# Performance work log

Hardware: AMD Instinct MI355X
Metric: run time of the kernel (lower is better)

Reference implementation:

```python
import jax, jax.numpy as jnp
import numpy as np

NEG_BIG = -9.0e15  # matches torch's -9000000000000000.0
LEAKY_SLOPE = 0.01  # nn.LeakyReLU default


def setup_inputs() -> dict:
    key = jax.random.key(0)
    k1, k2, k3, k4, k5, k6 = jax.random.split(key, 6)
    B, N, NEMB, NHID = 1, 8192, 128, 64
    x = jax.random.normal(k1, (B, N, NEMB), dtype=jnp.float32)
    adj = jax.random.randint(k2, (B, N, N), 0, 2, dtype=jnp.int32)
    # learned parameters (xavier-ish scale)
    w_weight = jax.random.normal(k3, (NHID, NEMB), dtype=jnp.float32) * (1.0 / np.sqrt(NEMB))
    w_bias = jnp.zeros((NHID,), dtype=jnp.float32)
    a_weight = jax.random.normal(k4, (1, 2 * NHID), dtype=jnp.float32) * (1.0 / np.sqrt(2 * NHID))
    a_bias = jnp.zeros((1,), dtype=jnp.float32)
    return {"x": x, "adj": adj, "w_weight": w_weight, "w_bias": w_bias,
            "a_weight": a_weight, "a_bias": a_bias}


def reference(x, adj, w_weight, w_bias, a_weight, a_bias):
    # h = W x + b : [B, N, F]
    h = jnp.einsum("bnd,fd->bnf", x, w_weight) + w_bias
    F = h.shape[-1]
    # The torch code forms a[b,i,j] = concat(h_i, h_j) then Linear(2F->1).
    # Equivalent decomposition avoids the [B,N,N,2F] tensor:
    # e[b,i,j] = leaky_relu(h_i . a_src + h_j . a_dst + a_bias)
    a_src, a_dst = a_weight[0, :F], a_weight[0, F:]
    s_src = jnp.einsum("bnf,f->bn", h, a_src)  # [B, N]
    s_dst = jnp.einsum("bnf,f->bn", h, a_dst)  # [B, N]
    e = jax.nn.leaky_relu(s_src[:, :, None] + s_dst[:, None, :] + a_bias[0],
                          negative_slope=LEAKY_SLOPE)  # [B, N, N]
    # masked_scatter_ semantics: True positions (row-major over the WHOLE
    # flattened tensor) receive e's elements taken sequentially in order.
    mask_flat = (adj > 0).reshape(-1)
    take_idx = jnp.cumsum(mask_flat.astype(jnp.int32)) - 1  # position in source stream
    src_flat = e.reshape(-1)
    att = jnp.where(mask_flat, src_flat[take_idx], jnp.float32(NEG_BIG)).reshape(e.shape)
    # softmax over dim=2, dropout in eval mode (identity)
    att = jax.nn.softmax(att, axis=2)
    out = jax.nn.elu(jnp.einsum("bij,bjf->bif", att, h))  # [B, N, F]
    return out
```

## Files before the change

### kernel.cpp

```cpp
#include <hip/hip_runtime.h>
#include <cstdint>
#include <cstddef>

#define N 8192
#define F 64
#define NEMB 128
#define BI 16
#define BJ 256
#define NCHUNK 32
#define HALFCH 16
#define ROWSTR 560
#define LEAKY 0.01f

typedef __attribute__((ext_vector_type(8))) short bf16x8;
typedef __attribute__((ext_vector_type(4))) float f32x4;

__device__ __forceinline__ float wave_reduce_sum_f(float v){
  #pragma unroll
  for (int d = 32; d > 0; d >>= 1) v += __shfl_xor(v, d, 64);
  return v;
}
__device__ __forceinline__ int wave_reduce_sum_i(int v){
  #pragma unroll
  for (int d = 32; d > 0; d >>= 1) v += __shfl_xor(v, d, 64);
  return v;
}
__device__ __forceinline__ int wave_incl_scan_i(int v, int lane){
  #pragma unroll
  for (int d = 1; d < 64; d <<= 1){
    int u = __shfl_up(v, d, 64);
    if (lane >= d) v += u;
  }
  return v;
}
__device__ __forceinline__ unsigned short f2bf(float x){
  union { float f; unsigned u; } v; v.f = x;
  unsigned r = v.u + 0x7fff + ((v.u >> 16) & 1);
  return (unsigned short)(r >> 16);
}

extern "C" __global__ void __launch_bounds__(256)
k_packh(const int* __restrict__ adj, unsigned short* __restrict__ bm,
        unsigned short* __restrict__ ccnt, int* __restrict__ rowtot,
        const float* __restrict__ x, const float* __restrict__ ww,
        const float* __restrict__ wb, const float* __restrict__ aw,
        float* __restrict__ h, float* __restrict__ ssrc, float* __restrict__ sdst2x){
  const int t = threadIdx.x;
  if (blockIdx.x < N){
    const int i = blockIdx.x;
    int total = 0;
    #pragma unroll
    for (int half = 0; half < 2; ++half){
      const int w = half*256 + t;
      const int4* p4 = (const int4*)(adj + (size_t)i*N + w*16);
      unsigned m = 0;
      #pragma unroll
      for (int k = 0; k < 4; ++k){
        int4 a = p4[k];
        m |= (unsigned)(a.x>0) << (k*4+0);
        m |= (unsigned)(a.y>0) << (k*4+1);
        m |= (unsigned)(a.z>0) << (k*4+2);
        m |= (unsigned)(a.w>0) << (k*4+3);
      }
      bm[((size_t)(w>>4)*N + i)*16 + (w&15)] = (unsigned short)m;
      const int pc = __popc(m);
      total += pc;
      int cs = pc;
      cs += __shfl_xor(cs, 1, 16);
      cs += __shfl_xor(cs, 2, 16);
      cs += __shfl_xor(cs, 4, 16);
      cs += __shfl_xor(cs, 8, 16);
      if ((t & 15) == 0) ccnt[(size_t)i*NCHUNK + (w>>4)] = (unsigned short)cs;
    }
    total = wave_reduce_sum_i(total);
    __shared__ int ws_[4];
    if ((t & 63) == 0) ws_[t >> 6] = total;
    __syncthreads();
    if (t == 0) rowtot[i] = ws_[0] + ws_[1] + ws_[2] + ws_[3];
  } else {
    const int w = t >> 6, lane = t & 63;
    __shared__ float xs[4][NEMB];
    const int n0 = (blockIdx.x - N) * 4;
    ((float2*)&xs[0][0])[t] = ((const float2*)(x + (size_t)n0 * NEMB))[t];
    __syncthreads();
    const int n = n0 + w;
    const float4* w4 = (const float4*)(ww + (size_t)lane * NEMB);
    const float4* x4 = (const float4*)&xs[w][0];
    float acc = wb[lane];
    #pragma unroll
    for (int k = 0; k < NEMB/4; ++k){
      float4 a = x4[k]; float4 b = w4[k];
      acc = fmaf(a.x, b.x, acc);
      acc = fmaf(a.y, b.y, acc);
      acc = fmaf(a.z, b.z, acc);
      acc = fmaf(a.w, b.w, acc);
    }
    h[(size_t)n * F + lane] = acc;
    float vs = wave_reduce_sum_f(acc * aw[lane]);
    float vd = wave_reduce_sum_f(acc * aw[F + lane]);
    if (lane == 0){ ssrc[n] = vs; sdst2x[n] = vd; sdst2x[n + N] = vd; }
  }
}

extern "C" __global__ void __launch_bounds__(256)
k_tr(const float* __restrict__ h, unsigned short* __restrict__ ht){
  __shared__ float tile[64][65];
  const int t = threadIdx.x;
  const int n0 = blockIdx.x * 64;
  #pragma unroll
  for (int s = 0; s < 4; ++s){
    const int r = s*16 + (t>>4);
    const int c = (t&15)*4;
    const float4 v = *(const float4*)(h + (size_t)(n0+r)*F + c);
    tile[r][c] = v.x; tile[r][c+1] = v.y; tile[r][c+2] = v.z; tile[r][c+3] = v.w;
  }
  __syncthreads();
  const int f = t >> 2, jq = t & 3;
  unsigned short buf[16];
  #pragma unroll
  for (int k = 0; k < 16; ++k) buf[k] = f2bf(tile[jq*16 + k][f]);
  *(uint4*)(ht + (size_t)f*N + n0 + jq*16)     = *(uint4*)&buf[0];
  *(uint4*)(ht + (size_t)f*N + n0 + jq*16 + 8) = *(uint4*)&buf[8];
}

extern "C" __global__ void __launch_bounds__(1024)
k_scan(const int* __restrict__ cnt, int* __restrict__ base){
  __shared__ int wsum[16];
  const int t = threadIdx.x, lane = t & 63, w = t >> 6;
  int4 aa = ((const int4*)cnt)[t * 2];
  int4 bb = ((const int4*)cnt)[t * 2 + 1];
  int v[8] = {aa.x, aa.y, aa.z, aa.w, bb.x, bb.y, bb.z, bb.w};
  int local = 0;
  #pragma unroll
  for (int k = 0; k < 8; ++k){ int tmp = v[k]; v[k] = local; local += tmp; }
  int inc = wave_incl_scan_i(local, lane);
  int wexcl = inc - local;
  if (lane == 63) wsum[w] = inc;
  __syncthreads();
  if (t == 0){
    int run = 0;
    #pragma unroll
    for (int k = 0; k < 16; ++k){ int tmp = wsum[k]; wsum[k] = run; run += tmp; }
  }
  __syncthreads();
  const int b0 = wsum[w] + wexcl;
  ((int4*)base)[t * 2]     = make_int4(b0 + v[0], b0 + v[1], b0 + v[2], b0 + v[3]);
  ((int4*)base)[t * 2 + 1] = make_int4(b0 + v[4], b0 + v[5], b0 + v[6], b0 + v[7]);
}

extern "C" __global__ void __launch_bounds__(256, 4)
k_main(const unsigned short* __restrict__ bm, const unsigned short* __restrict__ ccnt,
       const int* __restrict__ base, const unsigned short* __restrict__ ht,
       const float* __restrict__ ssrc, const float* __restrict__ sdst2x,
       const float* __restrict__ abias,
       float* __restrict__ pnum, float* __restrict__ pden){
  __shared__ __attribute__((aligned(16))) char pt[2][16*ROWSTR];
  __shared__ unsigned short ccum[BI][HALFCH];
  __shared__ int basel[BI];

  const int t = threadIdx.x, w = t >> 6, lane = t & 63;
  const int vid = blockIdx.x >> 1, half = blockIdx.x & 1;
  const int i0 = vid * BI;
  const int ch0 = half * HALFCH;

  if (t < BI) basel[t] = base[i0 + t];
  {
    const int r = t >> 4, g = t & 15;
    int c = (int)ccnt[(size_t)(i0+r)*NCHUNK + ch0 + g];
    int pre = 0;
    if (half){
      pre = (int)ccnt[(size_t)(i0+r)*NCHUNK + g];
      #pragma unroll
      for (int d = 1; d < 16; d <<= 1) pre += __shfl_xor(pre, d, 16);
    }
    int inc = c;
    #pragma unroll
    for (int d = 1; d < 16; d <<= 1){ int u = __shfl_up(inc, d, 16); if (g >= d) inc += u; }
    ccum[r][g] = (unsigned short)(pre + inc - c);
  }
  __syncthreads();

  const int r = t >> 4, g = t & 15;
  const int fr = lane & 15, ks = lane >> 4;
  const int fB = w*16 + fr;
  char* buf0 = pt[0];
  char* buf1 = pt[1];
  const float ab = abias[0];
  const int rowbase = basel[r];
  float dsum = 0.f;
  f32x4 acc = {0.f, 0.f, 0.f, 0.f};
  bf16x8 bregA[8], bregB[8];

#define PREFETCH(CH, BR) { \
    const unsigned short* hBp = ht + (size_t)fB*N + (CH)*BJ + ks*8; \
    _Pragma("unroll") \
    for (int kk = 0; kk < 8; ++kk) BR[kk] = *(const bf16x8*)(hBp + kk*32); \
    __builtin_amdgcn_sched_barrier(0); \
  }

#define PRODUCE(CC, PB) { \
    const int cc_ = (CC); \
    const int ch = ch0 + cc_; \
    const unsigned m = (unsigned)bm[((size_t)ch*N + (i0+r))*16 + g]; \
    const int c = __popc(m); \
    int inc = c; \
    _Pragma("unroll") \
    for (int d = 1; d < 16; d <<= 1){ int u = __shfl_up(inc, d, 16); if (g >= d) inc += u; } \
    const int qex = inc - c; \
    const int q0row = rowbase + (int)ccum[r][cc_]; \
    const float* sdw = sdst2x + (q0row & (N - 1)) + qex; \
    const int ilo = q0row >> 13; \
    const float s_lo = ssrc[ilo]; \
    const float s_hi = ssrc[ilo + 1]; \
    const int krel = ((ilo + 1) << 13) - q0row - qex; \
    char* myrow = (PB) + r*ROWSTR; \
    *(uint4*)(myrow + g*32)      = make_uint4(0,0,0,0); \
    *(uint4*)(myrow + g*32 + 16) = make_uint4(0,0,0,0); \
    float wv[16]; \
    _Pragma("unroll") \
    for (int k = 0; k < 16; ++k) wv[k] = sdw[k]; \
    unsigned mc = m; \
    _Pragma("unroll") \
    for (int k = 0; k < 16; ++k){ \
      const float ss = (k >= krel) ? s_hi : s_lo; \
      float e = ss + wv[k] + ab; \
      e = (e > 0.f) ? e : LEAKY * e; \
      const float p = __expf(e); \
      const int pos = __ffs(mc) - 1; \
      const bool act = (k < c); \
      dsum += act ? p : 0.f; \
      const int off = act ? (g*32 + pos*2) : (512 + g*2); \
      *(unsigned short*)(myrow + off) = f2bf(p); \
      mc &= mc - 1; \
    } \
  }

#define MM(PB, BR) { \
    const char* aP = (PB) + fr*ROWSTR; \
    __builtin_amdgcn_s_setprio(1); \
    _Pragma("unroll") \
    for (int kk = 0; kk < 8; ++kk){ \
      bf16x8 av = *(const bf16x8*)(aP + kk*64 + ks*16); \
      acc = __builtin_amdgcn_mfma_f32_16x16x32_bf16(av, BR[kk], acc, 0, 0, 0); \
    } \
    __builtin_amdgcn_s_setprio(0); \
  }

  PREFETCH(ch0, bregA)
  PRODUCE(0, buf0)
  __syncthreads();
  for (int cc = 0; cc < HALFCH; cc += 2){
    PREFETCH(ch0 + cc + 1, bregB)
    PRODUCE(cc + 1, buf1)
    MM(buf0, bregA)
    __syncthreads();
    if (cc + 2 < HALFCH){
      PREFETCH(ch0 + cc + 2, bregA)
      PRODUCE(cc + 2, buf0)
    }
    MM(buf1, bregB)
    __syncthreads();
  }
#undef PREFETCH
#undef PRODUCE
#undef MM

  #pragma unroll
  for (int d = 8; d > 0; d >>= 1) dsum += __shfl_xor(dsum, d, 16);
  if (g == 0) pden[(size_t)half*N + i0 + r] = dsum;
  #pragma unroll
  for (int reg = 0; reg < 4; ++reg){
    const int il = ks*4 + reg;
    pnum[(size_t)half*N*F + (size_t)(i0 + il)*F + fB] = acc[reg];
  }
}

extern "C" __global__ void __launch_bounds__(256)
k_comb(const float* __restrict__ pnum, const float* __restrict__ pden,
       float* __restrict__ out){
  const int idx = blockIdx.x * 256 + threadIdx.x;
  const int i = idx >> 6;
  const float dn = pden[i] + pden[N + i];
  const float nm = pnum[idx] + pnum[(size_t)N*F + idx];
  float v = (dn > 0.f) ? nm / dn : 0.f;
  out[idx] = (v > 0.f) ? v : (__expf(v) - 1.f);
}

extern "C" void kernel_launch(void* const* d_in, const int* in_sizes, int n_in,
                              void* d_out, int out_size, void* d_ws, size_t ws_size,
                              hipStream_t stream){
  const float* x   = (const float*)d_in[0];
  const int*   adj = (const int*)d_in[1];
  const float* ww  = (const float*)d_in[2];
  const float* wb  = (const float*)d_in[3];
  const float* aw  = (const float*)d_in[4];
  const float* ab  = (const float*)d_in[5];
  float* out = (float*)d_out;

  char* ws = (char*)d_ws;
  float*          h      = (float*)(ws);
  unsigned short* ht     = (unsigned short*)(ws + (2u<<20));
  float*          ssrc   = (float*)(ws + (3u<<20));
  float*          sdst2x = (float*)(ws + (3u<<20) + 32*1024);
  int*            rowtot = (int*)(ws + (3u<<20) + 96*1024);
  int*            base   = (int*)(ws + (3u<<20) + 128*1024);
  unsigned short* ccnt   = (unsigned short*)(ws + (3u<<20) + 160*1024);
  unsigned short* bm     = (unsigned short*)(ws + (4u<<20));
  float*          pnum   = (float*)(ws + (12u<<20));
  float*          pden   = (float*)(ws + (16u<<20));

  k_packh<<<N + N/4, 256, 0, stream>>>(adj, bm, ccnt, rowtot,
                                       x, ww, wb, aw, h, ssrc, sdst2x);
  k_tr  <<<N/64,   256, 0, stream>>>(h, ht);
  k_scan<<<1,     1024, 0, stream>>>(rowtot, base);
  k_main<<<2*(N/BI), 256, 0, stream>>>(bm, ccnt, base, ht, ssrc, sdst2x, ab, pnum, pden);
  k_comb<<<(N*F)/256, 256, 0, stream>>>(pnum, pden, out);
}
```

Baseline: 164.3 us.

## Software-pipeline bitmask loads and interleave MFMA with softmax producer in k_main

Splits the per-chunk producer into a load phase and a compute/store phase. The adjacency bitmask for the next chunk is now loaded one iteration ahead, and the MFMA on the previous buffer is placed between the gather loads and the exp/store work so memory latency overlaps with matrix math. It also folds the attention bias into ssrc inside k_packh, which removes one add per element in the inner loop. The cost is higher register pressure from keeping wv, the masks and two B-register sets live at once, which could hurt occupancy under launch_bounds(256,4).

```diff
diff --git a/kernel.cpp b/kernel.cpp
--- a/kernel.cpp
+++ b/kernel.cpp
@@ -44,6 +44,7 @@
         unsigned short* __restrict__ ccnt, int* __restrict__ rowtot,
         const float* __restrict__ x, const float* __restrict__ ww,
         const float* __restrict__ wb, const float* __restrict__ aw,
+        const float* __restrict__ abias,
         float* __restrict__ h, float* __restrict__ ssrc, float* __restrict__ sdst2x){
   const int t = threadIdx.x;
   if (blockIdx.x < N){
@@ -98,7 +99,10 @@
     h[(size_t)n * F + lane] = acc;
     float vs = wave_reduce_sum_f(acc * aw[lane]);
     float vd = wave_reduce_sum_f(acc * aw[F + lane]);
-    if (lane == 0){ ssrc[n] = vs; sdst2x[n] = vd; sdst2x[n + N] = vd; }
+    if (lane == 0){
+      ssrc[n] = vs + abias[0];
+      sdst2x[n] = vd; sdst2x[n + N] = vd;
+    }
   }
 }
 
@@ -152,7 +156,6 @@
 k_main(const unsigned short* __restrict__ bm, const unsigned short* __restrict__ ccnt,
        const int* __restrict__ base, const unsigned short* __restrict__ ht,
        const float* __restrict__ ssrc, const float* __restrict__ sdst2x,
-       const float* __restrict__ abias,
        float* __restrict__ pnum, float* __restrict__ pden){
   __shared__ __attribute__((aligned(16))) char pt[2][16*ROWSTR];
   __shared__ unsigned short ccum[BI][HALFCH];
@@ -164,8 +167,8 @@
   const int ch0 = half * HALFCH;
 
   if (t < BI) basel[t] = base[i0 + t];
+  const int r = t >> 4, g = t & 15;
   {
-    const int r = t >> 4, g = t & 15;
     int c = (int)ccnt[(size_t)(i0+r)*NCHUNK + ch0 + g];
     int pre = 0;
     if (half){
@@ -180,17 +183,17 @@
   }
   __syncthreads();
 
-  const int r = t >> 4, g = t & 15;
   const int fr = lane & 15, ks = lane >> 4;
   const int fB = w*16 + fr;
   char* buf0 = pt[0];
   char* buf1 = pt[1];
-  const float ab = abias[0];
   const int rowbase = basel[r];
   float dsum = 0.f;
   f32x4 acc = {0.f, 0.f, 0.f, 0.f};
   bf16x8 bregA[8], bregB[8];
 
+#define BMLD(CC) ((unsigned)bm[((size_t)(ch0 + (CC))*N + (i0 + r))*16 + g])
+
 #define PREFETCH(CH, BR) { \
     const unsigned short* hBp = ht + (size_t)fB*N + (CH)*BJ + ks*8; \
     _Pragma("unroll") \
@@ -198,16 +201,13 @@
     __builtin_amdgcn_sched_barrier(0); \
   }
 
-#define PRODUCE(CC, PB) { \
-    const int cc_ = (CC); \
-    const int ch = ch0 + cc_; \
-    const unsigned m = (unsigned)bm[((size_t)ch*N + (i0+r))*16 + g]; \
-    const int c = __popc(m); \
-    int inc = c; \
-    _Pragma("unroll") \
-    for (int d = 1; d < 16; d <<= 1){ int u = __shfl_up(inc, d, 16); if (g >= d) inc += u; } \
-    const int qex = inc - c; \
-    const int q0row = rowbase + (int)ccum[r][cc_]; \
+#define PLOAD(MV, CC, PB) \
+    const int c = __popc(MV); \
+    int inc_ = c; \
+    _Pragma("unroll") \
+    for (int d = 1; d < 16; d <<= 1){ int u = __shfl_up(inc_, d, 16); if (g >= d) inc_ += u; } \
+    const int qex = inc_ - c; \
+    const int q0row = rowbase + (int)ccum[r][CC]; \
     const float* sdw = sdst2x + (q0row & (N - 1)) + qex; \
     const int ilo = q0row >> 13; \
     const float s_lo = ssrc[ilo]; \
@@ -218,12 +218,14 @@
     *(uint4*)(myrow + g*32 + 16) = make_uint4(0,0,0,0); \
     float wv[16]; \
     _Pragma("unroll") \
-    for (int k = 0; k < 16; ++k) wv[k] = sdw[k]; \
-    unsigned mc = m; \
+    for (int k = 0; k < 16; ++k) wv[k] = sdw[k];
+
+#define PSTORE(MV) { \
+    unsigned mc = (MV); \
     _Pragma("unroll") \
     for (int k = 0; k < 16; ++k){ \
       const float ss = (k >= krel) ? s_hi : s_lo; \
-      float e = ss + wv[k] + ab; \
+      float e = ss + wv[k]; \
       e = (e > 0.f) ? e : LEAKY * e; \
       const float p = __expf(e); \
       const int pos = __ffs(mc) - 1; \
@@ -246,23 +248,40 @@
     __builtin_amdgcn_s_setprio(0); \
   }
 
-  PREFETCH(ch0, bregA)
-  PRODUCE(0, buf0)
-  __syncthreads();
+  unsigned mA = 0, mB = 0;
+  {
+    const unsigned m0 = BMLD(0);
+    mA = BMLD(1);
+    PREFETCH(ch0, bregA)
+    PLOAD(m0, 0, buf0)
+    PSTORE(m0)
+  }
+  __syncthreads();
+
   for (int cc = 0; cc < HALFCH; cc += 2){
-    PREFETCH(ch0 + cc + 1, bregB)
-    PRODUCE(cc + 1, buf1)
-    MM(buf0, bregA)
+    {
+      PLOAD(mA, cc + 1, buf1)
+      if (cc + 2 < HALFCH) mB = BMLD(cc + 2);
+      PREFETCH(ch0 + cc + 1, bregB)
+      MM(buf0, bregA)
+      PSTORE(mA)
+    }
     __syncthreads();
     if (cc + 2 < HALFCH){
+      PLOAD(mB, cc + 2, buf0)
+      if (cc + 3 < HALFCH) mA = BMLD(cc + 3);
       PREFETCH(ch0 + cc + 2, bregA)
-      PRODUCE(cc + 2, buf0)
-    }
-    MM(buf1, bregB)
+      MM(buf1, bregB)
+      PSTORE(mB)
+    } else {
+      MM(buf1, bregB)
+    }
     __syncthreads();
   }
+#undef BMLD
 #undef PREFETCH
-#undef PRODUCE
+#undef PLOAD
+#undef PSTORE
 #undef MM
 
   #pragma unroll
@@ -310,9 +329,9 @@
   float*          pden   = (float*)(ws + (16u<<20));
 
   k_packh<<<N + N/4, 256, 0, stream>>>(adj, bm, ccnt, rowtot,
-                                       x, ww, wb, aw, h, ssrc, sdst2x);
+                                       x, ww, wb, aw, ab, h, ssrc, sdst2x);
   k_tr  <<<N/64,   256, 0, stream>>>(h, ht);
   k_scan<<<1,     1024, 0, stream>>>(rowtot, base);
-  k_main<<<2*(N/BI), 256, 0, stream>>>(bm, ccnt, base, ht, ssrc, sdst2x, ab, pnum, pden);
+  k_main<<<2*(N/BI), 256, 0, stream>>>(bm, ccnt, base, ht, ssrc, sdst2x, pnum, pden);
   k_comb<<<(N*F)/256, 256, 0, stream>>>(pnum, pden, out);
 }
```

Result: slower. 196.9 us (+19.8%).
